# Kernel tuning notes

Hardware: AMD Instinct MI355X
Metric: run time of the kernel (lower is better)

The kernel has to match this reference:

```python
import jax, jax.numpy as jnp
import numpy as np

B, S, HID = 2, 2048, 4096
NH, NKV, HD = 32, 8, 128
GRP = NH // NKV          # query heads per kv head
G = 128                  # weight quant group size
FP8_MAX = 448.0          # e4m3 max
EPS = 1e-6


def _rmsnorm(x, w):
    return x * jax.lax.rsqrt(jnp.mean(x * x, axis=-1, keepdims=True) + EPS) * w


def _act_quant(x):
    # per-token fp8 quantization: scale = amax/448, values clipped to fp8 range
    s = jnp.max(jnp.abs(x), axis=-1, keepdims=True) / FP8_MAX
    s = jnp.maximum(s, 1e-6)
    return jnp.clip(x / s, -FP8_MAX, FP8_MAX), s


def _deq_weight(wi4, wscale):
    # wi4: [out, in] int values in [0,16) -> signed int4 [-8,7]
    # wscale: [out, in//G] per-group scales, broadcast along input dim
    return (wi4.astype(jnp.float32) - 8.0) * jnp.repeat(wscale, G, axis=1)


def _rotate_half(x):
    x1, x2 = jnp.split(x, 2, axis=-1)
    return jnp.concatenate([-x2, x1], axis=-1)


def setup_inputs() -> dict:
    key = jax.random.key(0)
    ks = jax.random.split(key, 8)
    hidden_states = jax.random.normal(ks[0], (B, S, HID), dtype=jnp.float32)
    ln_weight = jnp.ones((HID,), dtype=jnp.float32)
    # real RoPE tables
    inv_freq = 1.0 / (10000.0 ** (np.arange(0, HD, 2, dtype=np.float32) / HD))
    ang = np.arange(S, dtype=np.float32)[:, None] * inv_freq[None, :]
    emb = np.concatenate([ang, ang], axis=-1)  # [S, HD]
    cos = jnp.broadcast_to(jnp.asarray(np.cos(emb)), (B, S, HD)).astype(jnp.float32)
    sin = jnp.broadcast_to(jnp.asarray(np.sin(emb)), (B, S, HD)).astype(jnp.float32)
    def wq(k, out, inp):
        ki, ksc = jax.random.split(k)
        wi = jax.random.randint(ki, (out, inp), 0, 16, dtype=jnp.int32)
        sc = jax.random.uniform(ksc, (out, inp // G), dtype=jnp.float32) * 0.01 + 0.001
        return wi, sc
    wq_i4, wq_scale = wq(ks[1], NH * HD, HID)
    wk_i4, wk_scale = wq(ks[2], NKV * HD, HID)
    wv_i4, wv_scale = wq(ks[3], NKV * HD, HID)
    wo_i4, wo_scale = wq(ks[4], HID, NH * HD)
    return dict(hidden_states=hidden_states, ln_weight=ln_weight, cos=cos, sin=sin,
                wq_scale=wq_scale, wk_scale=wk_scale, wv_scale=wv_scale, wo_scale=wo_scale,
                wq_i4=wq_i4, wk_i4=wk_i4, wv_i4=wv_i4, wo_i4=wo_i4)


def reference(hidden_states, ln_weight, cos, sin,
              wq_scale, wk_scale, wv_scale, wo_scale,
              wq_i4, wk_i4, wv_i4, wo_i4):
    b, s, _ = hidden_states.shape
    residual = hidden_states
    h = _rmsnorm(hidden_states, ln_weight)
    qx, qx_s = _act_quant(h)                     # [b,s,HID], [b,s,1]
    q = (qx @ _deq_weight(wq_i4, wq_scale).T) * qx_s
    k = (qx @ _deq_weight(wk_i4, wk_scale).T) * qx_s
    v = (qx @ _deq_weight(wv_i4, wv_scale).T) * qx_s
    q = q.reshape(b, s, NH, HD)
    k = k.reshape(b, s, NKV, HD)
    v = v.reshape(b, s, NKV, HD)
    cse, sne = cos[:, :, None, :], sin[:, :, None, :]
    q = q * cse + _rotate_half(q) * sne
    k = k * cse + _rotate_half(k) * sne
    # GQA causal attention (fp8 fmha numerics emulated in fp32)
    qg = q.reshape(b, s, NKV, GRP, HD)
    scaling = HD ** -0.5
    scores = jnp.einsum('bskgd,btkd->bkgst', qg, k) * scaling  # [b,kv,g,s,t]
    causal = jnp.tril(jnp.ones((s, s), dtype=bool))
    scores = jnp.where(causal, scores, jnp.float32(-1e30))
    p = jax.nn.softmax(scores, axis=-1)
    o = jnp.einsum('bkgst,btkd->bskgd', p, v).reshape(b, s, NH * HD)
    qo, qo_s = _act_quant(o)
    out = (qo @ _deq_weight(wo_i4, wo_scale).T) * qo_s + residual
    return out
```

## Files before the change

### kernel.cpp

```cpp
#include <hip/hip_runtime.h>
#include <stdint.h>

#define HID    4096
#define SLEN   2048
#define BATCH  2
#define NHEADS 32
#define NKVH   8
#define HDIM   128
#define NTOK   (BATCH*SLEN)
#define NQK    (NHEADS*HDIM)
#define NKVD   (NKVH*HDIM)
#define NQKV   (NQK + 2*NKVD)
#define ASTR   (NQK + NKVD)

typedef unsigned short u16;
typedef short short8 __attribute__((ext_vector_type(8)));
typedef float f32x4 __attribute__((ext_vector_type(4)));
typedef int int4v __attribute__((ext_vector_type(4)));
typedef u16 u16x4 __attribute__((ext_vector_type(4)));

static __device__ __forceinline__ u16 f2bf(float f) {
  unsigned u = __builtin_bit_cast(unsigned, f);
  u += 0x7FFFu + ((u >> 16) & 1u);
  return (u16)(u >> 16);
}
static __device__ __forceinline__ float bf2f(u16 h) {
  return __builtin_bit_cast(float, (unsigned)h << 16);
}
static __device__ __forceinline__ void gload_lds16(const void* g, void* l) {
  __builtin_amdgcn_global_load_lds((const __attribute__((address_space(1))) void*)g,
                                   (__attribute__((address_space(3))) void*)l, 16, 0, 0);
}

__global__ __launch_bounds__(256) void k_rmsnorm(const float* __restrict__ x,
                                                 const float* __restrict__ w,
                                                 u16* __restrict__ h) {
  const int row = blockIdx.x;
  const float4* xr = (const float4*)(x + (size_t)row * HID);
  float4 vals[4];
  float ss = 0.f;
#pragma unroll
  for (int i = 0; i < 4; ++i) {
    float4 v = xr[threadIdx.x + i * 256];
    vals[i] = v;
    ss += v.x*v.x + v.y*v.y + v.z*v.z + v.w*v.w;
  }
#pragma unroll
  for (int off = 32; off; off >>= 1) ss += __shfl_xor(ss, off);
  __shared__ float red[4];
  if ((threadIdx.x & 63) == 0) red[threadIdx.x >> 6] = ss;
  __syncthreads();
  ss = red[0] + red[1] + red[2] + red[3];
  const float scale = rsqrtf(ss * (1.f / HID) + 1e-6f);
  u16* hr = h + (size_t)row * HID;
#pragma unroll
  for (int i = 0; i < 4; ++i) {
    int c = (threadIdx.x + i * 256) * 4;
    float4 v = vals[i];
    unsigned lo = (unsigned)f2bf(v.x * scale * w[c])   | ((unsigned)f2bf(v.y * scale * w[c+1]) << 16);
    unsigned hi = (unsigned)f2bf(v.z * scale * w[c+2]) | ((unsigned)f2bf(v.w * scale * w[c+3]) << 16);
    *(unsigned long long*)(hr + c) = ((unsigned long long)hi << 32) | lo;
  }
}

__global__ __launch_bounds__(256) void k_deq(const int* __restrict__ W,
                                             const float* __restrict__ Ws,
                                             u16* __restrict__ out) {
  const int idx = blockIdx.x * 256 + threadIdx.x;
  const int n = idx >> 9;
  const int k8 = (idx & 511) * 8;
  const float sc = Ws[n * 32 + (k8 >> 7)];
  int4v a = *(const int4v*)(W + (size_t)n * HID + k8);
  int4v b = *(const int4v*)(W + (size_t)n * HID + k8 + 4);
  u16 r[8];
#pragma unroll
  for (int j = 0; j < 4; ++j) r[j]     = f2bf((float)(a[j] - 8) * sc);
#pragma unroll
  for (int j = 0; j < 4; ++j) r[j + 4] = f2bf((float)(b[j] - 8) * sc);
  *(short8*)(out + (size_t)n * HID + k8) = *(short8*)r;
}

#define KD 4096
#define NT 64

#define STAGE_A_(nb, kt, mh)                                                   \
  { _Pragma("unroll") for (int r_ = 0; r_ < 2; ++r_) {                         \
      const int base_ = (mh)*64 + r_*128 + wave*8;                             \
      const int lr_ = base_ + (lane>>3);                                       \
      gload_lds16(Ag + (size_t)(m0 + lr_)*KD + (kt)*64 + (((lane&7) ^ (lr_&7))<<3), \
                  lA[nb] + base_*64); } }

#define STAGE_B_(nb, kt, nh)                                                   \
  { _Pragma("unroll") for (int r_ = 0; r_ < 2; ++r_) {                         \
      const int w8_ = r_*64 + wave*8;                                          \
      const int base_ = ((w8_>>5)<<6) + (nh)*32 + (w8_&31);                    \
      const int nr_ = base_ + (lane>>3);                                       \
      gload_lds16(Bg + (size_t)(n0 + nr_)*KD + (kt)*64 + (((lane&7) ^ (nr_&7))<<3), \
                  lB[nb] + base_*64); } }

#define DS_PHASE(buf, mh, nh)                                                  \
  { const int kb_ = lane >> 4;                                                 \
    _Pragma("unroll") for (int ks = 0; ks < 2; ++ks) {                         \
      _Pragma("unroll") for (int i = 0; i < 4; ++i) {                          \
        const int lr_ = wm*128 + (mh)*64 + i*16 + (lane & 15);                 \
        af[i][ks] = *(const short8*)(lA[buf] + lr_*64 + (((ks*4+kb_) ^ (lr_&7))<<3)); } \
      _Pragma("unroll") for (int j = 0; j < 2; ++j) {                          \
        const int nr_ = wn*64 + (nh)*32 + j*16 + (lane & 15);                  \
        bf[j][ks] = *(const short8*)(lB[buf] + nr_*64 + (((ks*4+kb_) ^ (nr_&7))<<3)); } } }

#define MFMA_PHASE(mh, nh)                                                     \
  __builtin_amdgcn_s_setprio(1);                                               \
  _Pragma("unroll") for (int ks = 0; ks < 2; ++ks)                             \
    _Pragma("unroll") for (int i = 0; i < 4; ++i)                              \
      _Pragma("unroll") for (int j = 0; j < 2; ++j)                            \
        acc[(mh)*4+i][(nh)*2+j] = __builtin_amdgcn_mfma_f32_16x16x32_bf16(     \
            af[i][ks], bf[j][ks], acc[(mh)*4+i][(nh)*2+j], 0, 0, 0);           \
  __builtin_amdgcn_s_setprio(0);

#define BAR()  __builtin_amdgcn_s_barrier(); asm volatile("" ::: "memory")
#define VMW(n) asm volatile("s_waitcnt vmcnt(" #n ")" ::: "memory")

#define GEMM8P_BODY                                                            \
  __shared__ __align__(16) u16 lA[2][256*64];                                  \
  __shared__ __align__(16) u16 lB[2][256*64];                                  \
  const int tid = threadIdx.x, lane = tid & 63, wave = tid >> 6;               \
  const int wm = wave >> 2, wn = wave & 3;                                     \
  f32x4 acc[8][4];                                                             \
  _Pragma("unroll") for (int mi = 0; mi < 8; ++mi)                             \
    _Pragma("unroll") for (int ni = 0; ni < 4; ++ni)                           \
      acc[mi][ni] = (f32x4){0.f, 0.f, 0.f, 0.f};                               \
  short8 af[4][2], bf[2][2];                                                   \
  STAGE_A_(0, 0, 0); STAGE_B_(0, 0, 0); STAGE_A_(0, 0, 1); STAGE_B_(0, 0, 1);  \
  VMW(4); BAR();                                                               \
  for (int t = 0; t < NT - 1; ++t) {                                           \
    const int cur = t & 1, nxt = cur ^ 1;                                      \
    DS_PHASE(cur, 0, 0);                                                       \
    STAGE_A_(nxt, t + 1, 0);                                                   \
    BAR();                                                                     \
    MFMA_PHASE(0, 0);                                                          \
    VMW(2); BAR();                                                             \
    DS_PHASE(cur, 0, 1);                                                       \
    STAGE_B_(nxt, t + 1, 0);                                                   \
    BAR();                                                                     \
    MFMA_PHASE(0, 1);                                                          \
    BAR();                                                                     \
    DS_PHASE(cur, 1, 0);                                                       \
    STAGE_A_(nxt, t + 1, 1);                                                   \
    BAR();                                                                     \
    MFMA_PHASE(1, 0);                                                          \
    BAR();                                                                     \
    DS_PHASE(cur, 1, 1);                                                       \
    STAGE_B_(nxt, t + 1, 1);                                                   \
    BAR();                                                                     \
    MFMA_PHASE(1, 1);                                                          \
    VMW(4); BAR();                                                             \
  }                                                                            \
  {                                                                            \
    const int cur = (NT - 1) & 1;                                              \
    DS_PHASE(cur, 0, 0);                                                       \
    BAR();                                                                     \
    MFMA_PHASE(0, 0);                                                          \
    VMW(0); BAR();                                                             \
    DS_PHASE(cur, 0, 1);                                                       \
    BAR();                                                                     \
    MFMA_PHASE(0, 1);                                                          \
    BAR();                                                                     \
    DS_PHASE(cur, 1, 0);                                                       \
    BAR();                                                                     \
    MFMA_PHASE(1, 0);                                                          \
    BAR();                                                                     \
    DS_PHASE(cur, 1, 1);                                                       \
    BAR();                                                                     \
    MFMA_PHASE(1, 1);                                                          \
  }

__global__ __launch_bounds__(512, 2) void k_gemm_qkv_8p(
    const u16* __restrict__ Ag, const u16* __restrict__ Bg,
    u16* __restrict__ C, u16* __restrict__ Vt) {
  const int wg = (blockIdx.x & 7) * 48 + (blockIdx.x >> 3);
  const int m0 = (wg & 15) * 256;
  const int n0 = (wg >> 4) * 256;
  GEMM8P_BODY
  if (n0 < ASTR) {
#pragma unroll
    for (int mi = 0; mi < 8; ++mi) {
      const int row = m0 + wm * 128 + mi * 16 + ((lane >> 4) << 2);
#pragma unroll
      for (int ni = 0; ni < 4; ++ni) {
        const int col = n0 + wn * 64 + ni * 16 + (lane & 15);
#pragma unroll
        for (int r = 0; r < 4; ++r)
          C[(size_t)(row + r) * ASTR + col] = f2bf(acc[mi][ni][r]);
      }
    }
  } else {
#pragma unroll
    for (int mi = 0; mi < 8; ++mi) {
      const int row = m0 + wm * 128 + mi * 16 + ((lane >> 4) << 2);
      const int b_ = row >> 11, s_ = row & 2047;
#pragma unroll
      for (int ni = 0; ni < 4; ++ni) {
        const int colv = (n0 - ASTR) + wn * 64 + ni * 16 + (lane & 15);
        u16x4 pk;
#pragma unroll
        for (int r = 0; r < 4; ++r) pk[r] = f2bf(acc[mi][ni][r]);
        *(u16x4*)(Vt + ((size_t)(b_ * NKVH + (colv >> 7)) * HDIM + (colv & 127)) * SLEN + s_) = pk;
      }
    }
  }
}

__global__ __launch_bounds__(512, 2) void k_gemm_o_8p(
    const u16* __restrict__ Ag, const u16* __restrict__ Bg,
    const float* __restrict__ resid, float* __restrict__ out) {
  const int wg = (blockIdx.x & 7) * 32 + (blockIdx.x >> 3);
  const int m0 = (wg & 15) * 256;
  const int n0 = (wg >> 4) * 256;
  GEMM8P_BODY
#pragma unroll
  for (int mi = 0; mi < 8; ++mi) {
    const int row = m0 + wm * 128 + mi * 16 + ((lane >> 4) << 2);
#pragma unroll
    for (int ni = 0; ni < 4; ++ni) {
      const int col = n0 + wn * 64 + ni * 16 + (lane & 15);
#pragma unroll
      for (int r = 0; r < 4; ++r) {
        const size_t idx = (size_t)(row + r) * HID + col;
        out[idx] = acc[mi][ni][r] + resid[idx];
      }
    }
  }
}

#define BM 128
#define BN 128
#define BK 64

__global__ __launch_bounds__(256) void k_gemm_qkv(
    const u16* __restrict__ A,
    const int* __restrict__ Wq, const int* __restrict__ Wk, const int* __restrict__ Wv,
    const float* __restrict__ Sq, const float* __restrict__ Sk, const float* __restrict__ Sv,
    u16* __restrict__ C, u16* __restrict__ Vt) {
  __shared__ __align__(16) u16 lA[BM * BK];
  __shared__ __align__(16) u16 lB[BN * BK];
  const int tid = threadIdx.x;
  const int lane = tid & 63;
  const int wave = tid >> 6;
  const int wm = wave >> 1, wn = wave & 1;
  const int m0 = blockIdx.x * BM;
  const int n0 = blockIdx.y * BN;

  const int* W; const float* Ws; int nb;
  if (n0 < NQK)       { W = Wq; Ws = Sq; nb = n0; }
  else if (n0 < ASTR) { W = Wk; Ws = Sk; nb = n0 - NQK; }
  else                { W = Wv; Ws = Sv; nb = n0 - ASTR; }

  const int mloc = wave * 8 + (lane >> 3);
  const int lb8 = (((lane & 7) ^ (lane >> 3)) << 3);

  f32x4 acc[4][4];
#pragma unroll
  for (int mi = 0; mi < 4; ++mi)
#pragma unroll
    for (int ni = 0; ni < 4; ++ni) acc[mi][ni] = (f32x4){0.f, 0.f, 0.f, 0.f};

  for (int k0 = 0; k0 < HID; k0 += BK) {
    __syncthreads();
#pragma unroll
    for (int p = 0; p < 4; ++p)
      gload_lds16(A + (size_t)(m0 + p * 32 + mloc) * HID + k0 + lb8,
                  lA + p * 2048 + wave * 512);
    const int grp = k0 >> 7;
#pragma unroll
    for (int p = 0; p < 8; ++p) {
      const int n = p * 16 + (tid >> 4);
      const int kk = (tid & 15) * 4;
      int4v wv4 = *(const int4v*)(W + (size_t)(nb + n) * HID + k0 + kk);
      const float sc = Ws[(nb + n) * 32 + grp];
      unsigned lo = (unsigned)f2bf((float)(wv4[0] - 8) * sc) |
                    ((unsigned)f2bf((float)(wv4[1] - 8) * sc) << 16);
      unsigned hi = (unsigned)f2bf((float)(wv4[2] - 8) * sc) |
                    ((unsigned)f2bf((float)(wv4[3] - 8) * sc) << 16);
      const int di = (n * 64 + kk) ^ ((n & 7) << 3);
      unsigned* dst = (unsigned*)(lB + di);
      dst[0] = lo; dst[1] = hi;
    }
    __syncthreads();
#pragma unroll
    for (int kc = 0; kc < 2; ++kc) {
      const int kOff = kc * 32 + ((lane >> 4) << 3);
      short8 af[4], bfr[4];
#pragma unroll
      for (int i = 0; i < 4; ++i) {
        const int m = wm * 64 + i * 16 + (lane & 15);
        af[i] = *(const short8*)(lA + ((m * 64 + kOff) ^ ((m & 7) << 3)));
        const int n = wn * 64 + i * 16 + (lane & 15);
        bfr[i] = *(const short8*)(lB + ((n * 64 + kOff) ^ ((n & 7) << 3)));
      }
#pragma unroll
      for (int mi = 0; mi < 4; ++mi)
#pragma unroll
        for (int ni = 0; ni < 4; ++ni)
          acc[mi][ni] = __builtin_amdgcn_mfma_f32_16x16x32_bf16(af[mi], bfr[ni], acc[mi][ni], 0, 0, 0);
    }
  }
  if (n0 < ASTR) {
#pragma unroll
    for (int mi = 0; mi < 4; ++mi) {
      const int row = m0 + wm * 64 + mi * 16 + ((lane >> 4) << 2);
#pragma unroll
      for (int ni = 0; ni < 4; ++ni) {
        const int col = n0 + wn * 64 + ni * 16 + (lane & 15);
#pragma unroll
        for (int r = 0; r < 4; ++r)
          C[(size_t)(row + r) * ASTR + col] = f2bf(acc[mi][ni][r]);
      }
    }
  } else {
#pragma unroll
    for (int mi = 0; mi < 4; ++mi) {
      const int row = m0 + wm * 64 + mi * 16 + ((lane >> 4) << 2);
      const int b_ = row >> 11, s_ = row & 2047;
#pragma unroll
      for (int ni = 0; ni < 4; ++ni) {
        const int colv = (n0 - ASTR) + wn * 64 + ni * 16 + (lane & 15);
        u16x4 pk;
#pragma unroll
        for (int r = 0; r < 4; ++r) pk[r] = f2bf(acc[mi][ni][r]);
        *(u16x4*)(Vt + ((size_t)(b_ * NKVH + (colv >> 7)) * HDIM + (colv & 127)) * SLEN + s_) = pk;
      }
    }
  }
}

__global__ __launch_bounds__(256) void k_gemm_o(
    const u16* __restrict__ A, const int* __restrict__ W, const float* __restrict__ Ws,
    const float* __restrict__ resid, float* __restrict__ out) {
  __shared__ __align__(16) u16 lA[BM * BK];
  __shared__ __align__(16) u16 lB[BN * BK];
  const int tid = threadIdx.x;
  const int lane = tid & 63;
  const int wave = tid >> 6;
  const int wm = wave >> 1, wn = wave & 1;
  const int m0 = blockIdx.x * BM;
  const int n0 = blockIdx.y * BN;

  const int mloc = wave * 8 + (lane >> 3);
  const int lb8 = (((lane & 7) ^ (lane >> 3)) << 3);

  f32x4 acc[4][4];
#pragma unroll
  for (int mi = 0; mi < 4; ++mi)
#pragma unroll
    for (int ni = 0; ni < 4; ++ni) acc[mi][ni] = (f32x4){0.f, 0.f, 0.f, 0.f};

  for (int k0 = 0; k0 < NQK; k0 += BK) {
    __syncthreads();
#pragma unroll
    for (int p = 0; p < 4; ++p)
      gload_lds16(A + (size_t)(m0 + p * 32 + mloc) * NQK + k0 + lb8,
                  lA + p * 2048 + wave * 512);
    const int grp = k0 >> 7;
#pragma unroll
    for (int p = 0; p < 8; ++p) {
      const int n = p * 16 + (tid >> 4);
      const int kk = (tid & 15) * 4;
      int4v wv4 = *(const int4v*)(W + (size_t)(n0 + n) * NQK + k0 + kk);
      const float sc = Ws[(n0 + n) * 32 + grp];
      unsigned lo = (unsigned)f2bf((float)(wv4[0] - 8) * sc) |
                    ((unsigned)f2bf((float)(wv4[1] - 8) * sc) << 16);
      unsigned hi = (unsigned)f2bf((float)(wv4[2] - 8) * sc) |
                    ((unsigned)f2bf((float)(wv4[3] - 8) * sc) << 16);
      const int di = (n * 64 + kk) ^ ((n & 7) << 3);
      unsigned* dst = (unsigned*)(lB + di);
      dst[0] = lo; dst[1] = hi;
    }
    __syncthreads();
#pragma unroll
    for (int kc = 0; kc < 2; ++kc) {
      const int kOff = kc * 32 + ((lane >> 4) << 3);
      short8 af[4], bfr[4];
#pragma unroll
      for (int i = 0; i < 4; ++i) {
        const int m = wm * 64 + i * 16 + (lane & 15);
        af[i] = *(const short8*)(lA + ((m * 64 + kOff) ^ ((m & 7) << 3)));
        const int n = wn * 64 + i * 16 + (lane & 15);
        bfr[i] = *(const short8*)(lB + ((n * 64 + kOff) ^ ((n & 7) << 3)));
      }
#pragma unroll
      for (int mi = 0; mi < 4; ++mi)
#pragma unroll
        for (int ni = 0; ni < 4; ++ni)
          acc[mi][ni] = __builtin_amdgcn_mfma_f32_16x16x32_bf16(af[mi], bfr[ni], acc[mi][ni], 0, 0, 0);
      }
  }
#pragma unroll
  for (int mi = 0; mi < 4; ++mi) {
    const int row = m0 + wm * 64 + mi * 16 + ((lane >> 4) << 2);
#pragma unroll
    for (int ni = 0; ni < 4; ++ni) {
      const int col = n0 + wn * 64 + ni * 16 + (lane & 15);
#pragma unroll
      for (int r = 0; r < 4; ++r) {
        const size_t idx = (size_t)(row + r) * HID + col;
        out[idx] = acc[mi][ni][r] + resid[idx];
      }
    }
  }
}

__global__ __launch_bounds__(256) void k_rope(u16* __restrict__ qk,
                                              const float* __restrict__ cosb,
                                              const float* __restrict__ sinb) {
  const int idx = blockIdx.x * 256 + threadIdx.x;
  const int d = idx & 63;
  const int hh = (idx >> 6) % 40;
  const int t = idx / (64 * 40);
  const int col = (hh < 32) ? hh * HDIM : NQK + (hh - 32) * HDIM;
  u16* p = qk + (size_t)t * ASTR + col;
  const float c = cosb[t * HDIM + d], s = sinb[t * HDIM + d];
  const float x1 = bf2f(p[d]), x2 = bf2f(p[d + 64]);
  p[d]      = f2bf(x1 * c - x2 * s);
  p[d + 64] = f2bf(x2 * c + x1 * s);
}

__global__ __launch_bounds__(256) void k_attn(const u16* __restrict__ qk,
                                              const u16* __restrict__ vt,
                                              u16* __restrict__ o) {
  const int slot = blockIdx.x;
  const int w = (slot & 7) * 128 + (slot >> 3);
  const int qi = 15 - (w & 15);
  const int h = (w >> 4) & 31;
  const int b = w >> 9;
  const int kvh = h >> 2;
  const int q0 = qi * 128;
  const int lane = threadIdx.x & 63, wave = threadIdx.x >> 6;
  const int m = lane & 15, kg = lane >> 4;

  const u16* Qb = qk + (size_t)b * SLEN * ASTR + h * HDIM;
  const u16* Kb = qk + (size_t)b * SLEN * ASTR + NQK + kvh * HDIM;
  const u16* Vb = vt + (size_t)(b * NKVH + kvh) * HDIM * SLEN;

  __shared__ __align__(16) u16 Kt[64 * 128];
  __shared__ __align__(16) u16 Vts[128 * 64];
  __shared__ __align__(16) u16 Pl[4][32 * 72];

  const int qr = q0 + wave * 32;
  short8 qf[2][4];
#pragma unroll
  for (int mi = 0; mi < 2; ++mi)
#pragma unroll
    for (int kc = 0; kc < 4; ++kc)
      qf[mi][kc] = *(const short8*)(Qb + (size_t)(qr + mi * 16 + m) * ASTR + kc * 32 + kg * 8);

  f32x4 oacc[2][8];
#pragma unroll
  for (int mi = 0; mi < 2; ++mi)
#pragma unroll
    for (int n = 0; n < 8; ++n) oacc[mi][n] = (f32x4){0.f, 0.f, 0.f, 0.f};
  float rm[2][4], rl[2][4];
#pragma unroll
  for (int mi = 0; mi < 2; ++mi)
#pragma unroll
    for (int r = 0; r < 4; ++r) { rm[mi][r] = -3.0e38f; rl[mi][r] = 0.f; }

  const float sscale = 0.08838834764831845f;
  const int nt = q0 / 64 + 2;
  for (int t = 0; t < nt; ++t) {
    const int kv0 = t * 64;
    __syncthreads();
#pragma unroll
    for (int p = 0; p < 4; ++p) {
      const int row = p * 16 + wave * 4 + (lane >> 4);
      const int c8s = (lane & 15) ^ (row & 7);
      gload_lds16(Kb + (size_t)(kv0 + row) * ASTR + c8s * 8, Kt + p * 2048 + wave * 512);
    }
#pragma unroll
    for (int p = 0; p < 4; ++p) {
      const int d = p * 32 + wave * 8 + (lane >> 3);
      const int c8s = (lane & 7) ^ (d & 7);
      gload_lds16(Vb + (size_t)d * SLEN + kv0 + c8s * 8, Vts + p * 2048 + wave * 512);
    }
    __syncthreads();

    f32x4 sf[2][4];
#pragma unroll
    for (int mi = 0; mi < 2; ++mi)
#pragma unroll
      for (int ni = 0; ni < 4; ++ni) sf[mi][ni] = (f32x4){0.f, 0.f, 0.f, 0.f};
#pragma unroll
    for (int ni = 0; ni < 4; ++ni)
#pragma unroll
      for (int kc = 0; kc < 4; ++kc) {
        const int krow = ni * 16 + m;
        short8 kf = *(const short8*)(Kt + krow * 128 + (((kc * 4 + kg) ^ (krow & 7)) << 3));
#pragma unroll
        for (int mi = 0; mi < 2; ++mi)
          sf[mi][ni] = __builtin_amdgcn_mfma_f32_16x16x32_bf16(qf[mi][kc], kf, sf[mi][ni], 0, 0, 0);
      }

#pragma unroll
    for (int mi = 0; mi < 2; ++mi) {
      const bool dg = (kv0 + 63 > qr + mi * 16);
      float tmax[4] = {-3.0e38f, -3.0e38f, -3.0e38f, -3.0e38f};
#pragma unroll
      for (int ni = 0; ni < 4; ++ni)
#pragma unroll
        for (int r = 0; r < 4; ++r) {
          float s = sf[mi][ni][r] * sscale;
          if (dg) {
            const int rowg = qr + mi * 16 + kg * 4 + r;
            const int colg = kv0 + ni * 16 + m;
            if (colg > rowg) s = -1e30f;
          }
          sf[mi][ni][r] = s;
          tmax[r] = fmaxf(tmax[r], s);
        }
#pragma unroll
      for (int r = 0; r < 4; ++r)
#pragma unroll
        for (int off = 1; off < 16; off <<= 1)
          tmax[r] = fmaxf(tmax[r], __shfl_xor(tmax[r], off));
      float scl[4], psum[4];
#pragma unroll
      for (int r = 0; r < 4; ++r) {
        const float mn = fmaxf(rm[mi][r], tmax[r]);
        scl[r] = __expf(rm[mi][r] - mn);
        rm[mi][r] = mn;
        psum[r] = 0.f;
      }
#pragma unroll
      for (int ni = 0; ni < 4; ++ni)
#pragma unroll
        for (int r = 0; r < 4; ++r) {
          const float p = __expf(sf[mi][ni][r] - rm[mi][r]);
          psum[r] += p;
          Pl[wave][(mi * 16 + kg * 4 + r) * 72 + ni * 16 + m] = f2bf(p);
        }
#pragma unroll
      for (int r = 0; r < 4; ++r) {
#pragma unroll
        for (int off = 1; off < 16; off <<= 1)
          psum[r] += __shfl_xor(psum[r], off);
        rl[mi][r] = rl[mi][r] * scl[r] + psum[r];
      }
#pragma unroll
      for (int n = 0; n < 8; ++n)
#pragma unroll
        for (int r = 0; r < 4; ++r) oacc[mi][n][r] *= scl[r];
    }

#pragma unroll
    for (int kc = 0; kc < 2; ++kc) {
      short8 pf[2];
#pragma unroll
      for (int mi = 0; mi < 2; ++mi)
        pf[mi] = *(const short8*)(&Pl[wave][(mi * 16 + m) * 72 + kc * 32 + kg * 8]);
#pragma unroll
      for (int n = 0; n < 8; ++n) {
        const int vrow = n * 16 + m;
        short8 vf = *(const short8*)(Vts + vrow * 64 + (((kc * 4 + kg) ^ (vrow & 7)) << 3));
#pragma unroll
        for (int mi = 0; mi < 2; ++mi)
          oacc[mi][n] = __builtin_amdgcn_mfma_f32_16x16x32_bf16(pf[mi], vf, oacc[mi][n], 0, 0, 0);
      }
    }
  }

#pragma unroll
  for (int mi = 0; mi < 2; ++mi) {
    float inv[4];
#pragma unroll
    for (int r = 0; r < 4; ++r) inv[r] = 1.0f / rl[mi][r];
#pragma unroll
    for (int n = 0; n < 8; ++n)
#pragma unroll
      for (int r = 0; r < 4; ++r) {
        const int row = qr + mi * 16 + kg * 4 + r;
        o[((size_t)b * SLEN + row) * NQK + h * HDIM + n * 16 + m] = f2bf(oacc[mi][n][r] * inv[r]);
      }
  }
}

extern "C" void kernel_launch(void* const* d_in, const int* in_sizes, int n_in,
                              void* d_out, int out_size, void* d_ws, size_t ws_size,
                              hipStream_t stream) {
  (void)in_sizes; (void)n_in; (void)out_size;
  const float* x    = (const float*)d_in[0];
  const float* lnw  = (const float*)d_in[1];
  const float* cosb = (const float*)d_in[2];
  const float* sinb = (const float*)d_in[3];
  const float* sq   = (const float*)d_in[4];
  const float* sk   = (const float*)d_in[5];
  const float* sv   = (const float*)d_in[6];
  const float* so   = (const float*)d_in[7];
  const int* wq     = (const int*)d_in[8];
  const int* wk     = (const int*)d_in[9];
  const int* wv     = (const int*)d_in[10];
  const int* wo     = (const int*)d_in[11];

  u16* h   = (u16*)d_ws;
  u16* qkb = h + (size_t)NTOK * HID;
  u16* vtb = qkb + (size_t)NTOK * ASTR;
  u16* wqkvb = vtb + (size_t)BATCH * NKVH * HDIM * SLEN;
  u16* wob   = wqkvb + (size_t)NQKV * HID;
  float* out = (float*)d_out;

  const size_t need = ((size_t)NTOK * HID + (size_t)NTOK * ASTR +
                       (size_t)BATCH * NKVH * HDIM * SLEN +
                       (size_t)NQKV * HID + (size_t)HID * NQK) * sizeof(u16);
  const bool predeq = (ws_size >= need);

  k_rmsnorm<<<NTOK, 256, 0, stream>>>(x, lnw, h);

  if (predeq) {
    k_deq<<<NQK  * 2, 256, 0, stream>>>(wq, sq, wqkvb);
    k_deq<<<NKVD * 2, 256, 0, stream>>>(wk, sk, wqkvb + (size_t)NQK * HID);
    k_deq<<<NKVD * 2, 256, 0, stream>>>(wv, sv, wqkvb + (size_t)ASTR * HID);
    k_deq<<<NQK  * 2, 256, 0, stream>>>(wo, so, wob);
    k_gemm_qkv_8p<<<384, 512, 0, stream>>>(h, wqkvb, qkb, vtb);
  } else {
    dim3 g1(NTOK / BM, NQKV / BN);
    k_gemm_qkv<<<g1, 256, 0, stream>>>(h, wq, wk, wv, sq, sk, sv, qkb, vtb);
  }

  k_rope<<<(NTOK * 40 * 64) / 256, 256, 0, stream>>>(qkb, cosb, sinb);

  k_attn<<<1024, 256, 0, stream>>>(qkb, vtb, h);

  if (predeq) {
    k_gemm_o_8p<<<256, 512, 0, stream>>>(h, wob, x, out);
  } else {
    dim3 g3(NTOK / BM, HID / BN);
    k_gemm_o<<<g3, 256, 0, stream>>>(h, wo, so, x, out);
  }
}
```

Baseline: 755.9 us.

## Merge four weight-dequant launches and restructure GEMM pipeline into unrolled half-tile stages

The four per-matrix dequantization kernels become one launch that picks the source matrix by row index, relying on wob directly following wqkvb in the workspace. The GEMM main loop is unrolled by two k-tiles with fixed buffer indices, and the staging of the next tile's half-panels is shifted earlier so loads are issued one phase ahead. This cuts launch overhead and aims to hide global-to-LDS latency better. The new buffer indexing and wait counts add a risk of LDS read/write hazards.

```diff
diff --git a/kernel.cpp b/kernel.cpp
--- a/kernel.cpp
+++ b/kernel.cpp
@@ -63,21 +63,29 @@
   }
 }
 
-__global__ __launch_bounds__(256) void k_deq(const int* __restrict__ W,
-                                             const float* __restrict__ Ws,
-                                             u16* __restrict__ out) {
+__global__ __launch_bounds__(256) void k_deq_all(
+    const int* __restrict__ wq, const int* __restrict__ wk,
+    const int* __restrict__ wv, const int* __restrict__ wo,
+    const float* __restrict__ sq, const float* __restrict__ sk,
+    const float* __restrict__ sv, const float* __restrict__ so,
+    u16* __restrict__ out) {
   const int idx = blockIdx.x * 256 + threadIdx.x;
-  const int n = idx >> 9;
+  const int row = idx >> 9;
   const int k8 = (idx & 511) * 8;
-  const float sc = Ws[n * 32 + (k8 >> 7)];
-  int4v a = *(const int4v*)(W + (size_t)n * HID + k8);
-  int4v b = *(const int4v*)(W + (size_t)n * HID + k8 + 4);
-  u16 r[8];
-#pragma unroll
-  for (int j = 0; j < 4; ++j) r[j]     = f2bf((float)(a[j] - 8) * sc);
-#pragma unroll
-  for (int j = 0; j < 4; ++j) r[j + 4] = f2bf((float)(b[j] - 8) * sc);
-  *(short8*)(out + (size_t)n * HID + k8) = *(short8*)r;
+  const int* W; const float* S; int r;
+  if (row < 4096)      { W = wq; S = sq; r = row; }
+  else if (row < 5120) { W = wk; S = sk; r = row - 4096; }
+  else if (row < 6144) { W = wv; S = sv; r = row - 5120; }
+  else                 { W = wo; S = so; r = row - 6144; }
+  const float sc = S[r * 32 + (k8 >> 7)];
+  int4v a = *(const int4v*)(W + (size_t)r * HID + k8);
+  int4v b = *(const int4v*)(W + (size_t)r * HID + k8 + 4);
+  u16 rr[8];
+#pragma unroll
+  for (int j = 0; j < 4; ++j) rr[j]     = f2bf((float)(a[j] - 8) * sc);
+#pragma unroll
+  for (int j = 0; j < 4; ++j) rr[j + 4] = f2bf((float)(b[j] - 8) * sc);
+  *(short8*)(out + (size_t)row * HID + k8) = *(short8*)rr;
 }
 
 #define KD 4096
@@ -130,49 +138,32 @@
     _Pragma("unroll") for (int ni = 0; ni < 4; ++ni)                           \
       acc[mi][ni] = (f32x4){0.f, 0.f, 0.f, 0.f};                               \
   short8 af[4][2], bf[2][2];                                                   \
+                   \
   STAGE_A_(0, 0, 0); STAGE_B_(0, 0, 0); STAGE_A_(0, 0, 1); STAGE_B_(0, 0, 1);  \
+  STAGE_A_(1, 1, 0); STAGE_B_(1, 1, 0);                                        \
   VMW(4); BAR();                                                               \
-  for (int t = 0; t < NT - 1; ++t) {                                           \
-    const int cur = t & 1, nxt = cur ^ 1;                                      \
-    DS_PHASE(cur, 0, 0);                                                       \
-    STAGE_A_(nxt, t + 1, 0);                                                   \
-    BAR();                                                                     \
-    MFMA_PHASE(0, 0);                                                          \
-    VMW(2); BAR();                                                             \
-    DS_PHASE(cur, 0, 1);                                                       \
-    STAGE_B_(nxt, t + 1, 0);                                                   \
-    BAR();                                                                     \
-    MFMA_PHASE(0, 1);                                                          \
-    BAR();                                                                     \
-    DS_PHASE(cur, 1, 0);                                                       \
-    STAGE_A_(nxt, t + 1, 1);                                                   \
-    BAR();                                                                     \
-    MFMA_PHASE(1, 0);                                                          \
-    BAR();                                                                     \
-    DS_PHASE(cur, 1, 1);                                                       \
-    STAGE_B_(nxt, t + 1, 1);                                                   \
-    BAR();                                                                     \
-    MFMA_PHASE(1, 1);                                                          \
+  for (int it = 0; it < NT/2 - 1; ++it) {                                      \
+    const int k1 = 2*it + 1, k2 = 2*it + 2, k3 = 2*it + 3;                     \
+    DS_PHASE(0, 0, 0); STAGE_A_(1, k1, 1); BAR(); MFMA_PHASE(0, 0); BAR();     \
+    DS_PHASE(0, 0, 1); STAGE_B_(1, k1, 1); BAR(); MFMA_PHASE(0, 1); BAR();     \
+    DS_PHASE(0, 1, 0); STAGE_A_(0, k2, 0); BAR(); MFMA_PHASE(1, 0); BAR();     \
+    DS_PHASE(0, 1, 1); STAGE_B_(0, k2, 0); BAR(); MFMA_PHASE(1, 1);            \
+    VMW(4); BAR();                                                             \
+    DS_PHASE(1, 0, 0); STAGE_A_(0, k2, 1); BAR(); MFMA_PHASE(0, 0); BAR();     \
+    DS_PHASE(1, 0, 1); STAGE_B_(0, k2, 1); BAR(); MFMA_PHASE(0, 1); BAR();     \
+    DS_PHASE(1, 1, 0); STAGE_A_(1, k3, 0); BAR(); MFMA_PHASE(1, 0); BAR();     \
+    DS_PHASE(1, 1, 1); STAGE_B_(1, k3, 0); BAR(); MFMA_PHASE(1, 1);            \
     VMW(4); BAR();                                                             \
   }                                                                            \
-  {                                                                            \
-    const int cur = (NT - 1) & 1;                                              \
-    DS_PHASE(cur, 0, 0);                                                       \
-    BAR();                                                                     \
-    MFMA_PHASE(0, 0);                                                          \
-    VMW(0); BAR();                                                             \
-    DS_PHASE(cur, 0, 1);                                                       \
-    BAR();                                                                     \
-    MFMA_PHASE(0, 1);                                                          \
-    BAR();                                                                     \
-    DS_PHASE(cur, 1, 0);                                                       \
-    BAR();                                                                     \
-    MFMA_PHASE(1, 0);                                                          \
-    BAR();                                                                     \
-    DS_PHASE(cur, 1, 1);                                                       \
-    BAR();                                                                     \
-    MFMA_PHASE(1, 1);                                                          \
-  }
+    \
+  DS_PHASE(0, 0, 0); STAGE_A_(1, NT-1, 1); BAR(); MFMA_PHASE(0, 0); BAR();     \
+  DS_PHASE(0, 0, 1); STAGE_B_(1, NT-1, 1); BAR(); MFMA_PHASE(0, 1); BAR();     \
+  DS_PHASE(0, 1, 0); BAR(); MFMA_PHASE(1, 0); BAR();                           \
+  DS_PHASE(0, 1, 1); BAR(); MFMA_PHASE(1, 1); VMW(0); BAR();                   \
+  DS_PHASE(1, 0, 0); BAR(); MFMA_PHASE(0, 0); BAR();                           \
+  DS_PHASE(1, 0, 1); BAR(); MFMA_PHASE(0, 1); BAR();                           \
+  DS_PHASE(1, 1, 0); BAR(); MFMA_PHASE(1, 0); BAR();                           \
+  DS_PHASE(1, 1, 1); BAR(); MFMA_PHASE(1, 1);
 
 __global__ __launch_bounds__(512, 2) void k_gemm_qkv_8p(
     const u16* __restrict__ Ag, const u16* __restrict__ Bg,
@@ -614,10 +605,7 @@
   k_rmsnorm<<<NTOK, 256, 0, stream>>>(x, lnw, h);
 
   if (predeq) {
-    k_deq<<<NQK  * 2, 256, 0, stream>>>(wq, sq, wqkvb);
-    k_deq<<<NKVD * 2, 256, 0, stream>>>(wk, sk, wqkvb + (size_t)NQK * HID);
-    k_deq<<<NKVD * 2, 256, 0, stream>>>(wv, sv, wqkvb + (size_t)ASTR * HID);
-    k_deq<<<NQK  * 2, 256, 0, stream>>>(wo, so, wob);
+    k_deq_all<<<(10240 * 512) / 256, 256, 0, stream>>>(wq, wk, wv, wo, sq, sk, sv, so, wqkvb);
     k_gemm_qkv_8p<<<384, 512, 0, stream>>>(h, wqkvb, qkb, vtb);
   } else {
     dim3 g1(NTOK / BM, NQKV / BN);
```

Result: slower. 838.6 us (+10.9%).
